# Kernel optimization log

Hardware: AMD Instinct MI355X
Metric: run time of the kernel (lower is better)

Reference implementation:

```python
import jax, jax.numpy as jnp
import numpy as np

CLASSES = (16, 16)
CH_IN = 128
CH_LAT = 128
B, H, W = 1, 192, 256


def setup_inputs() -> dict:
    key = jax.random.key(0)
    ks = jax.random.split(key, 20)

    def w(k, shape, fan_in):
        return (jax.random.normal(k, shape, jnp.float32) / np.float32(np.sqrt(fan_in)))

    c0, c1 = CLASSES
    inp = {
        "x_in": jax.random.normal(ks[0], (B, CH_IN, H, W), jnp.float32),
        # 1x1 convs: weight [out, in], bias [out]
        "w_c11": w(ks[1], (CH_LAT, CH_IN), CH_IN), "b_c11": 0.01 * jax.random.normal(ks[2], (CH_LAT,), jnp.float32),
        "w_c12": w(ks[3], (CH_LAT, CH_LAT), CH_LAT), "b_c12": 0.01 * jax.random.normal(ks[4], (CH_LAT,), jnp.float32),
        "w_c13": w(ks[5], (c0 + 1, CH_LAT), CH_LAT), "b_c13": 0.01 * jax.random.normal(ks[6], (c0 + 1,), jnp.float32),
        # CondMul: weight [n_classes, in, out], bias [n_classes, out]
        "w_c21": w(ks[7], (c0, CH_IN, 32), CH_IN), "b_c21": 0.01 * jax.random.normal(ks[8], (c0, 32), jnp.float32),
        "w_c22": w(ks[9], (c0, 32, 32), 32), "b_c22": 0.01 * jax.random.normal(ks[10], (c0, 32), jnp.float32),
        "w_c23": w(ks[11], (c0, 32, c1), 32), "b_c23": 0.01 * jax.random.normal(ks[12], (c0, c1), jnp.float32),
        "w_r11": w(ks[13], (c0 * c1, CH_IN, 32), CH_IN), "b_r11": 0.01 * jax.random.normal(ks[14], (c0 * c1, 32), jnp.float32),
        "w_r12": w(ks[15], (c0 * c1, 32, 16), 32), "b_r12": 0.01 * jax.random.normal(ks[16], (c0 * c1, 16), jnp.float32),
        "w_r13": w(ks[17], (c0 * c1, 16, 1), 16), "b_r13": 0.01 * jax.random.normal(ks[18], (c0 * c1, 1), jnp.float32),
    }
    return inp


def _conv1x1(x, w, b):
    # x: [B,C,H,W], w: [O,C] -> [B,O,H,W]
    return jnp.einsum('bchw,oc->bohw', x, w) + b[None, :, None, None]


def _cond_mul(x, inds, w, b):
    # x: [N,in], inds: [N] int32, w: [C,in,out], b: [C,out] -> [N,out]
    return jnp.einsum('ni,nio->no', x, w[inds]) + b[inds]


def reference(x_in, w_c11, b_c11, w_c12, b_c12, w_c13, b_c13,
              w_c21, b_c21, w_c22, b_c22, w_c23, b_c23,
              w_r11, b_r11, w_r12, b_r12, w_r13, b_r13):
    lrelu = jax.nn.leaky_relu  # negative_slope=0.01, matches F.leaky_relu default
    c0, c1 = CLASSES
    total = c0 * c1

    x1 = lrelu(_conv1x1(x_in, w_c11, b_c11))
    x1 = lrelu(_conv1x1(x1, w_c12, b_c12))
    x1 = _conv1x1(x1, w_c13, b_c13)  # [B, c0+1, H, W]
    mask = lrelu(x1[:, -1:, :, :])

    # coarse routing: argmax over class logits, flattened in (B,H,W) order as in torch
    inds1 = jnp.argmax(x1[:, :c0], axis=1).reshape(-1).astype(jnp.int32)

    # tokens flattened via transpose(1,3): (B,W,H) order, faithful to original
    tok = jnp.transpose(x_in, (0, 3, 2, 1)).reshape(-1, x_in.shape[1])  # [N, CH_IN]

    x2 = lrelu(_cond_mul(tok, inds1, w_c21, b_c21))
    x2 = lrelu(_cond_mul(x2, inds1, w_c22, b_c22))
    x2 = _cond_mul(x2, inds1, w_c23, b_c23)  # [N, c1]

    inds2 = jnp.argmax(x2, axis=1).astype(jnp.int32)
    inds12 = inds1 * c0 + inds2  # original multiplies by classes[0]

    x3 = lrelu(_cond_mul(tok, inds12, w_r11, b_r11))
    x3 = lrelu(_cond_mul(x3, inds12, w_r12, b_r12))
    r = _cond_mul(x3, inds12, w_r13, b_r13).reshape(-1)  # [N]

    x_real = (inds12.astype(jnp.float32) + r) * (1.0 / float(total))
    x_real = x_real.reshape(x_in.shape[0], 1, x_in.shape[2], x_in.shape[3])
    return x_real, mask
```

## Files before the change

### kernel.cpp

```cpp
#include <hip/hip_runtime.h>

#define NPIX 49152
#define H_ 192
#define W_ 256
#define TPB 64

__global__ __launch_bounds__(256) void wtrans2_k(const float* __restrict__ Wa,
    float* __restrict__ WTa, const float* __restrict__ Wb,
    float* __restrict__ WTb, int* __restrict__ S) {
  const int b = blockIdx.x;
  const float* __restrict__ W = (b < 16) ? Wa : Wb;
  float* __restrict__ WT = (b < 16) ? WTa : WTb;
  const int bb = b & 15;
  __shared__ float tile[32][33];
  const int bx = bb & 3, by = bb >> 2;
  const int c = threadIdx.x & 31, r0 = threadIdx.x >> 5;
#pragma unroll
  for (int j = 0; j < 4; ++j) {
    const int r = r0 + j * 8;
    tile[r][c] = W[(by * 32 + r) * 128 + bx * 32 + c];
  }
  __syncthreads();
#pragma unroll
  for (int j = 0; j < 4; ++j) {
    const int r = r0 + j * 8;
    WT[(bx * 32 + r) * 128 + by * 32 + c] = tile[c][r];
  }
  if (b == 0) {
    const int t = threadIdx.x;
    if (t < 32) S[t] = 0;
    S[1088 + t] = 0;
    S[1344 + t] = 0;
  }
}

__global__ __launch_bounds__(512) void convfused_k(const float* __restrict__ X,
    const float* __restrict__ WT1, const float* __restrict__ Bv1,
    const float* __restrict__ WT2, const float* __restrict__ Bv2,
    const float* __restrict__ W3, const float* __restrict__ Bv3,
    unsigned char* __restrict__ inds1, float* __restrict__ mask_out,
    int* __restrict__ cnt1, float* __restrict__ xt) {
  __shared__ float xs2[128][65];
  __shared__ float w3s[128 * 20];
  __shared__ int lh[16];
  const int t = threadIdx.x;
  const int px = t & 63;
  const int p0 = blockIdx.x * 64;
  int ob = (t >> 6) * 16;
  ob = __builtin_amdgcn_readfirstlane(ob);
  if (t < 16) lh[t] = 0;

  {
    float xr[16];
#pragma unroll
    for (int kk = 0; kk < 16; ++kk)
      xr[kk] = X[(ob + kk) * NPIX + p0 + px];
#pragma unroll
    for (int kk = 0; kk < 16; ++kk)
      xs2[ob + kk][px] = xr[kk];
  }
  __syncthreads();

  float acc[16];

  const float* __restrict__ W1u = WT1 + ob;
#pragma unroll
  for (int o = 0; o < 16; ++o) acc[o] = Bv1[ob + o];
#pragma unroll 8
  for (int k = 0; k < 128; ++k) {
    const float xv = xs2[k][px];
#pragma unroll
    for (int o = 0; o < 16; ++o)
      acc[o] = fmaf(xv, W1u[k * 128 + o], acc[o]);
  }

#pragma unroll
  for (int i = 0; i < 4; ++i) {
    const int idx = t * 4 + i;
    const int tok = idx >> 5, c4 = idx & 31;
    const int pg = p0 + tok;
    float4 v;
    v.x = xs2[c4 * 4 + 0][tok];
    v.y = xs2[c4 * 4 + 1][tok];
    v.z = xs2[c4 * 4 + 2][tok];
    v.w = xs2[c4 * 4 + 3][tok];
    *(float4*)(xt + ((pg & 255) * H_ + (pg >> 8)) * 128 + c4 * 4) = v;
  }
  __syncthreads();

#pragma unroll
  for (int o = 0; o < 16; ++o) {
    const float v = acc[o];
    xs2[ob + o][px] = v > 0.f ? v : 0.01f * v;
  }
  __syncthreads();

  const float* __restrict__ W2u = WT2 + ob;
#pragma unroll
  for (int o = 0; o < 16; ++o) acc[o] = Bv2[ob + o];
#pragma unroll 8
  for (int k = 0; k < 128; ++k) {
    const float xv = xs2[k][px];
#pragma unroll
    for (int o = 0; o < 16; ++o)
      acc[o] = fmaf(xv, W2u[k * 128 + o], acc[o]);
  }
  __syncthreads();

#pragma unroll
  for (int o = 0; o < 16; ++o) {
    const float v = acc[o];
    xs2[ob + o][px] = v > 0.f ? v : 0.01f * v;
  }
  for (int i = t; i < 17 * 128; i += 512)
    w3s[(i & 127) * 20 + (i >> 7)] = W3[i];
  __syncthreads();

  {
    const int p = t >> 3, s = t & 7;
    float s2[2];
    s2[0] = Bv3[2 * s];
    s2[1] = Bv3[2 * s + 1];
    float m = Bv3[16];
#pragma unroll 8
    for (int k = 0; k < 128; ++k) {
      const float xv = xs2[k][p];
      float2 w2 = *(const float2*)&w3s[k * 20 + 2 * s];
      s2[0] = fmaf(xv, w2.x, s2[0]);
      s2[1] = fmaf(xv, w2.y, s2[1]);
      m = fmaf(xv, w3s[k * 20 + 16], m);
    }
    float bv = s2[0];
    int bi = 2 * s;
    if (s2[1] > bv) { bv = s2[1]; bi = 2 * s + 1; }
#pragma unroll
    for (int d = 1; d < 8; d <<= 1) {
      const float ov = __shfl_xor(bv, d, 64);
      const int oi = __shfl_xor(bi, d, 64);
      if (ov > bv || (ov == bv && oi < bi)) { bv = ov; bi = oi; }
    }
    if (s == 0) {
      inds1[p0 + p] = (unsigned char)bi;
      mask_out[p0 + p] = m > 0.f ? m : 0.01f * m;
      atomicAdd(&lh[bi], 1);
    }
  }
  __syncthreads();
  if (t < 16 && lh[t] > 0) atomicAdd(&cnt1[t], lh[t]);
}

template<int NB>
__global__ __launch_bounds__(256) void scan_desc_k(const int* __restrict__ cnt,
    int* __restrict__ off, int* __restrict__ desc, int* __restrict__ ndesc) {
  const int t = threadIdx.x;
  const int lane = t & 63, wvi = t >> 6;
  __shared__ int wsumC[4], wsumD[4];
  const int c = (t < NB) ? cnt[t] : 0;
  const int nb = (c + TPB - 1) / TPB;
  int ic = c, id = nb;
  for (int d = 1; d < 64; d <<= 1) {
    const int uc = __shfl_up(ic, d, 64);
    const int ud = __shfl_up(id, d, 64);
    if (lane >= d) { ic += uc; id += ud; }
  }
  if (lane == 63) { wsumC[wvi] = ic; wsumD[wvi] = id; }
  __syncthreads();
  int bc = 0, bd = 0;
#pragma unroll
  for (int w2 = 0; w2 < 4; ++w2) {
    if (w2 < wvi) { bc += wsumC[w2]; bd += wsumD[w2]; }
  }
  ic += bc; id += bd;
  if (t < NB) {
    off[t] = ic - c;
    const int db = id - nb;
    for (int j = 0; j < nb; ++j) desc[db + j] = (t << 12) | j;
  }
  if (t == NB - 1) *ndesc = id;
}

template<typename T>
__global__ __launch_bounds__(256) void scatter_k(const T* __restrict__ bins,
    const int* __restrict__ off, int* __restrict__ cursor,
    int* __restrict__ ord, int nbins) {
  __shared__ int lhist[256], lbase[256], lcur[256];
  const int t = threadIdx.x;
  const int n = blockIdx.x * 256 + t;
  if (t < nbins) { lhist[t] = 0; lcur[t] = 0; }
  __syncthreads();
  const int b = (int)bins[n];
  atomicAdd(&lhist[b], 1);
  __syncthreads();
  if (t < nbins && lhist[t] > 0) lbase[t] = atomicAdd(&cursor[t], lhist[t]);
  __syncthreads();
  const int r = atomicAdd(&lcur[b], 1);
  ord[off[b] + lbase[b] + r] = n;
}

__global__ __launch_bounds__(256) void chain1_k(const float* __restrict__ xt,
    const int* __restrict__ ord1, const int* __restrict__ off1,
    const int* __restrict__ cnt1, const int* __restrict__ desc1,
    const int* __restrict__ nd1,
    const float* __restrict__ wc21, const float* __restrict__ bc21,
    const float* __restrict__ wc22, const float* __restrict__ bc22,
    const float* __restrict__ wc23, const float* __restrict__ bc23,
    int* __restrict__ e12a, int* __restrict__ cnt2) {
  if ((int)blockIdx.x >= *nd1) return;
  __shared__ float w1s[4096];
  __shared__ float w2s[1024];
  __shared__ float w3s[512];
  __shared__ float bs[80];
  __shared__ float xs_[64][132];
  __shared__ int lh[16];
  const int t = threadIdx.x;
  if (t < 16) lh[t] = 0;
  const int tg = t >> 2, sub = t & 3;
  const int l0 = (t & 63) & ~3;
  const int de = desc1[blockIdx.x];
  const int e = de >> 12, chunk = de & 0xFFF;
  const int cnt = cnt1[e];
  const int pos = chunk * TPB + tg;
  const bool valid = pos < cnt;
  const int n = valid ? ord1[off1[e] + pos] : 0;

  {
    const float4* __restrict__ Wg1 = (const float4*)(wc21 + e * 4096);
#pragma unroll
    for (int j = 0; j < 4; ++j)
      *(float4*)&w1s[t * 4 + j * 1024] = Wg1[t + j * 256];
    const float4* __restrict__ Wg2 = (const float4*)(wc22 + e * 1024);
    *(float4*)&w2s[t * 4] = Wg2[t];
    if (t < 128) {
      const float4* __restrict__ Wg3 = (const float4*)(wc23 + e * 512);
      *(float4*)&w3s[t * 4] = Wg3[t];
    }
    if (t < 32) bs[t] = bc21[e * 32 + t];
    else if (t < 64) bs[t] = bc22[e * 32 + (t - 32)];
    else if (t < 80) bs[t] = bc23[e * 16 + (t - 64)];
  }
  {
    const float4* __restrict__ src = (const float4*)(xt + n * 128 + sub * 32);
    float4 tmp[8];
#pragma unroll
    for (int j = 0; j < 8; ++j) tmp[j] = src[j];
#pragma unroll
    for (int j = 0; j < 8; ++j)
      *(float4*)(&xs_[tg][sub * 32 + 4 * j]) = tmp[j];
  }
  __syncthreads();

  const int wb1 = sub * 8;
  float a[8];
#pragma unroll
  for (int o = 0; o < 8; ++o) a[o] = bs[wb1 + o];
#pragma unroll
  for (int k = 0; k < 128; k += 4) {
    float x4[4];
    *(float4*)x4 = *(const float4*)(&xs_[tg][k]);
#pragma unroll
    for (int kk = 0; kk < 4; ++kk) {
      float w8[8];
      *(float4*)&w8[0] = *(const float4*)&w1s[(k + kk) * 32 + wb1];
      *(float4*)&w8[4] = *(const float4*)&w1s[(k + kk) * 32 + wb1 + 4];
#pragma unroll
      for (int o = 0; o < 8; ++o) a[o] = fmaf(x4[kk], w8[o], a[o]);
    }
  }
#pragma unroll
  for (int o = 0; o < 8; ++o) a[o] = a[o] > 0.f ? a[o] : 0.01f * a[o];

  float b[8];
#pragma unroll
  for (int o = 0; o < 8; ++o) b[o] = bs[32 + wb1 + o];
#pragma unroll
  for (int i = 0; i < 32; ++i) {
    const float hv = __shfl(a[i & 7], l0 + (i >> 3), 64);
    float w8[8];
    *(float4*)&w8[0] = *(const float4*)&w2s[i * 32 + wb1];
    *(float4*)&w8[4] = *(const float4*)&w2s[i * 32 + wb1 + 4];
#pragma unroll
    for (int o = 0; o < 8; ++o) b[o] = fmaf(hv, w8[o], b[o]);
  }
#pragma unroll
  for (int o = 0; o < 8; ++o) b[o] = b[o] > 0.f ? b[o] : 0.01f * b[o];

  float s[4];
#pragma unroll
  for (int j = 0; j < 4; ++j) s[j] = bs[64 + sub * 4 + j];
#pragma unroll
  for (int i = 0; i < 32; ++i) {
    const float hv = __shfl(b[i & 7], l0 + (i >> 3), 64);
    float w4[4];
    *(float4*)w4 = *(const float4*)&w3s[i * 16 + sub * 4];
#pragma unroll
    for (int j = 0; j < 4; ++j) s[j] = fmaf(hv, w4[j], s[j]);
  }

  float bv = s[0];
  int bi = sub * 4;
#pragma unroll
  for (int j = 1; j < 4; ++j) {
    if (s[j] > bv) { bv = s[j]; bi = sub * 4 + j; }
  }
#pragma unroll
  for (int d = 1; d < 4; d <<= 1) {
    const float ov = __shfl_xor(bv, d, 64);
    const int oi = __shfl_xor(bi, d, 64);
    if (ov > bv || (ov == bv && oi < bi)) { bv = ov; bi = oi; }
  }
  const int e12 = e * 16 + bi;
  if (valid && sub == 0) {
    e12a[n] = e12;
    atomicAdd(&lh[bi], 1);
  }
  __syncthreads();
  if (t < 16 && lh[t] > 0)
    atomicAdd(&cnt2[e * 16 + t], lh[t]);
}

__global__ __launch_bounds__(256) void chain2_k(const float* __restrict__ xt,
    const int* __restrict__ ord2, const int* __restrict__ off2,
    const int* __restrict__ cnt2, const int* __restrict__ desc2,
    const int* __restrict__ nd2,
    const float* __restrict__ wr11, const float* __restrict__ br11,
    const float* __restrict__ wr12, const float* __restrict__ br12,
    const float* __restrict__ wr13, const float* __restrict__ br13,
    float* __restrict__ out) {
  if ((int)blockIdx.x >= *nd2) return;
  __shared__ float w1s[4096];
  __shared__ float w2s[512];
  __shared__ float w3s[16];
  __shared__ float bs[49];
  __shared__ float xs_[64][132];
  const int t = threadIdx.x;
  const int tg = t >> 2, sub = t & 3;
  const int l0 = (t & 63) & ~3;
  const int de = desc2[blockIdx.x];
  const int e12 = de >> 12, chunk = de & 0xFFF;
  const int cnt = cnt2[e12];
  const int pos = chunk * TPB + tg;
  const bool valid = pos < cnt;
  const int n = valid ? ord2[off2[e12] + pos] : 0;

  {
    const float4* __restrict__ Wg1 = (const float4*)(wr11 + e12 * 4096);
#pragma unroll
    for (int j = 0; j < 4; ++j)
      *(float4*)&w1s[t * 4 + j * 1024] = Wg1[t + j * 256];
    if (t < 128) {
      const float4* __restrict__ Wg2 = (const float4*)(wr12 + e12 * 512);
      *(float4*)&w2s[t * 4] = Wg2[t];
    }
    if (t < 16) w3s[t] = wr13[e12 * 16 + t];
    if (t < 32) bs[t] = br11[e12 * 32 + t];
    else if (t < 48) bs[t] = br12[e12 * 16 + (t - 32)];
    else if (t == 48) bs[48] = br13[e12];
  }
  {
    const float4* __restrict__ src = (const float4*)(xt + n * 128 + sub * 32);
    float4 tmp[8];
#pragma unroll
    for (int j = 0; j < 8; ++j) tmp[j] = src[j];
#pragma unroll
    for (int j = 0; j < 8; ++j)
      *(float4*)(&xs_[tg][sub * 32 + 4 * j]) = tmp[j];
  }
  __syncthreads();

  const int wb1 = sub * 8;
  float a[8];
#pragma unroll
  for (int o = 0; o < 8; ++o) a[o] = bs[wb1 + o];
#pragma unroll
  for (int k = 0; k < 128; k += 4) {
    float x4[4];
    *(float4*)x4 = *(const float4*)(&xs_[tg][k]);
#pragma unroll
    for (int kk = 0; kk < 4; ++kk) {
      float w8[8];
      *(float4*)&w8[0] = *(const float4*)&w1s[(k + kk) * 32 + wb1];
      *(float4*)&w8[4] = *(const float4*)&w1s[(k + kk) * 32 + wb1 + 4];
#pragma unroll
      for (int o = 0; o < 8; ++o) a[o] = fmaf(x4[kk], w8[o], a[o]);
    }
  }
#pragma unroll
  for (int o = 0; o < 8; ++o) a[o] = a[o] > 0.f ? a[o] : 0.01f * a[o];

  float s[4];
#pragma unroll
  for (int j = 0; j < 4; ++j) s[j] = bs[32 + sub * 4 + j];
#pragma unroll
  for (int i = 0; i < 32; ++i) {
    const float hv = __shfl(a[i & 7], l0 + (i >> 3), 64);
    float w4[4];
    *(float4*)w4 = *(const float4*)&w2s[i * 16 + sub * 4];
#pragma unroll
    for (int j = 0; j < 4; ++j) s[j] = fmaf(hv, w4[j], s[j]);
  }
#pragma unroll
  for (int j = 0; j < 4; ++j) s[j] = s[j] > 0.f ? s[j] : 0.01f * s[j];

  float r = bs[48];
#pragma unroll
  for (int i = 0; i < 16; ++i) {
    const float hv = __shfl(s[i & 3], l0 + (i >> 2), 64);
    r = fmaf(hv, w3s[i], r);
  }

  if (valid && sub == 0) out[n] = ((float)e12 + r) * (1.0f / 256.0f);
}

extern "C" void kernel_launch(void* const* d_in, const int* in_sizes, int n_in,
                              void* d_out, int out_size, void* d_ws,
                              size_t ws_size, hipStream_t stream) {
  const float* x_in  = (const float*)d_in[0];
  const float* w_c11 = (const float*)d_in[1];
  const float* b_c11 = (const float*)d_in[2];
  const float* w_c12 = (const float*)d_in[3];
  const float* b_c12 = (const float*)d_in[4];
  const float* w_c13 = (const float*)d_in[5];
  const float* b_c13 = (const float*)d_in[6];
  const float* w_c21 = (const float*)d_in[7];
  const float* b_c21 = (const float*)d_in[8];
  const float* w_c22 = (const float*)d_in[9];
  const float* b_c22 = (const float*)d_in[10];
  const float* w_c23 = (const float*)d_in[11];
  const float* b_c23 = (const float*)d_in[12];
  const float* w_r11 = (const float*)d_in[13];
  const float* b_r11 = (const float*)d_in[14];
  const float* w_r12 = (const float*)d_in[15];
  const float* b_r12 = (const float*)d_in[16];
  const float* w_r13 = (const float*)d_in[17];
  const float* b_r13 = (const float*)d_in[18];

  float* out = (float*)d_out;

  float* R0 = (float*)d_ws;
  float* R1 = R0 + 128 * NPIX;
  float* R2 = R1 + 128 * NPIX;

  float* xt = R0;
  unsigned char* inds1 = (unsigned char*)R2;
  float* wT1 = R2 + 12288;
  float* wT2 = wT1 + 16384;
  int* S = (int*)R2 + 45056;

  int* cnt1  = S;
  int* cur1  = S + 16;
  int* off1  = S + 32;
  int* nd1   = S + 48;
  int* desc1 = S + 64;
  int* cnt2  = S + 1088;
  int* cur2  = S + 1344;
  int* off2  = S + 1600;
  int* nd2   = S + 1856;
  int* desc2 = S + 1872;

  int* ib   = (int*)R1;
  int* ord1 = ib;
  int* ord2 = ib + NPIX;
  int* e12a = ib + 2 * NPIX;

  wtrans2_k<<<32, 256, 0, stream>>>(w_c11, wT1, w_c12, wT2, S);
  convfused_k<<<NPIX / 64, 512, 0, stream>>>(x_in, wT1, b_c11, wT2, b_c12,
      w_c13, b_c13, inds1, out + NPIX, cnt1, xt);
  scan_desc_k<16><<<1, 256, 0, stream>>>(cnt1, off1, desc1, nd1);
  scatter_k<unsigned char><<<NPIX / 256, 256, 0, stream>>>(inds1, off1, cur1,
                                                           ord1, 16);
  chain1_k<<<NPIX / TPB + 16, 256, 0, stream>>>(xt, ord1, off1, cnt1, desc1,
      nd1, w_c21, b_c21, w_c22, b_c22, w_c23, b_c23, e12a, cnt2);
  scan_desc_k<256><<<1, 256, 0, stream>>>(cnt2, off2, desc2, nd2);
  scatter_k<int><<<NPIX / 256, 256, 0, stream>>>(e12a, off2, cur2, ord2, 256);
  chain2_k<<<NPIX / TPB + 256, 256, 0, stream>>>(xt, ord2, off2, cnt2, desc2,
      nd2, w_r11, b_r11, w_r12, b_r12, w_r13, b_r13, out);
}
```

Measured before the change: 123.0 us.

## Restructure cond-MLP kernels to wave-uniform weight loads with transposed token tiles

Both routed MLP kernels now map one token per lane and one output slice per wavefront. Because the wave index is made uniform with readfirstlane, weights can be read straight from global memory as scalar loads instead of being staged into LDS. Activations move between layers through padded transposed LDS tiles, which replaces the cross-lane shuffles. This cuts the LDS footprint and the per-block weight staging, at the cost of more barriers and a serial 16-way argmax done by a single wave.

```diff
diff --git a/kernel.cpp b/kernel.cpp
--- a/kernel.cpp
+++ b/kernel.cpp
@@ -206,112 +206,103 @@
     const float* __restrict__ wc23, const float* __restrict__ bc23,
     int* __restrict__ e12a, int* __restrict__ cnt2) {
   if ((int)blockIdx.x >= *nd1) return;
-  __shared__ float w1s[4096];
-  __shared__ float w2s[1024];
-  __shared__ float w3s[512];
-  __shared__ float bs[80];
-  __shared__ float xs_[64][132];
+  __shared__ float xs_t[128][65];
+  __shared__ float actA[32][65];
+  __shared__ float actB[32][65];
   __shared__ int lh[16];
   const int t = threadIdx.x;
   if (t < 16) lh[t] = 0;
-  const int tg = t >> 2, sub = t & 3;
-  const int l0 = (t & 63) & ~3;
+  const int tok = t & 63;
+  int w = t >> 6;
+  w = __builtin_amdgcn_readfirstlane(w);
   const int de = desc1[blockIdx.x];
   const int e = de >> 12, chunk = de & 0xFFF;
   const int cnt = cnt1[e];
-  const int pos = chunk * TPB + tg;
+  const int pos = chunk * TPB + tok;
   const bool valid = pos < cnt;
   const int n = valid ? ord1[off1[e] + pos] : 0;
 
   {
-    const float4* __restrict__ Wg1 = (const float4*)(wc21 + e * 4096);
+    const float4* __restrict__ src = (const float4*)(xt + n * 128 + w * 32);
+    float4 tmp[8];
+#pragma unroll
+    for (int j = 0; j < 8; ++j) tmp[j] = src[j];
+#pragma unroll
+    for (int j = 0; j < 8; ++j) {
+      const float* v = (const float*)&tmp[j];
+#pragma unroll
+      for (int c = 0; c < 4; ++c)
+        xs_t[w * 32 + j * 4 + c][tok] = v[c];
+    }
+  }
+  __syncthreads();
+
+  const float* __restrict__ W1u = wc21 + e * 4096 + w * 8;
+  const float* __restrict__ B1u = bc21 + e * 32 + w * 8;
+  float a[8];
+#pragma unroll
+  for (int o = 0; o < 8; ++o) a[o] = B1u[o];
+#pragma unroll 8
+  for (int k = 0; k < 128; ++k) {
+    const float xv = xs_t[k][tok];
+#pragma unroll
+    for (int o = 0; o < 8; ++o)
+      a[o] = fmaf(xv, W1u[k * 32 + o], a[o]);
+  }
+#pragma unroll
+  for (int o = 0; o < 8; ++o) {
+    const float v = a[o] > 0.f ? a[o] : 0.01f * a[o];
+    actA[w * 8 + o][tok] = v;
+  }
+  __syncthreads();
+
+  const float* __restrict__ W2u = wc22 + e * 1024 + w * 8;
+  const float* __restrict__ B2u = bc22 + e * 32 + w * 8;
+  float b[8];
+#pragma unroll
+  for (int o = 0; o < 8; ++o) b[o] = B2u[o];
+#pragma unroll 8
+  for (int i = 0; i < 32; ++i) {
+    const float hv = actA[i][tok];
+#pragma unroll
+    for (int o = 0; o < 8; ++o)
+      b[o] = fmaf(hv, W2u[i * 32 + o], b[o]);
+  }
+#pragma unroll
+  for (int o = 0; o < 8; ++o) {
+    const float v = b[o] > 0.f ? b[o] : 0.01f * b[o];
+    actB[w * 8 + o][tok] = v;
+  }
+  __syncthreads();
+
+  const float* __restrict__ W3u = wc23 + e * 512 + w * 4;
+  const float* __restrict__ B3u = bc23 + e * 16 + w * 4;
+  float s[4];
+#pragma unroll
+  for (int j = 0; j < 4; ++j) s[j] = B3u[j];
+#pragma unroll 8
+  for (int i = 0; i < 32; ++i) {
+    const float hv = actB[i][tok];
 #pragma unroll
     for (int j = 0; j < 4; ++j)
-      *(float4*)&w1s[t * 4 + j * 1024] = Wg1[t + j * 256];
-    const float4* __restrict__ Wg2 = (const float4*)(wc22 + e * 1024);
-    *(float4*)&w2s[t * 4] = Wg2[t];
-    if (t < 128) {
-      const float4* __restrict__ Wg3 = (const float4*)(wc23 + e * 512);
-      *(float4*)&w3s[t * 4] = Wg3[t];
-    }
-    if (t < 32) bs[t] = bc21[e * 32 + t];
-    else if (t < 64) bs[t] = bc22[e * 32 + (t - 32)];
-    else if (t < 80) bs[t] = bc23[e * 16 + (t - 64)];
-  }
-  {
-    const float4* __restrict__ src = (const float4*)(xt + n * 128 + sub * 32);
-    float4 tmp[8];
-#pragma unroll
-    for (int j = 0; j < 8; ++j) tmp[j] = src[j];
-#pragma unroll
-    for (int j = 0; j < 8; ++j)
-      *(float4*)(&xs_[tg][sub * 32 + 4 * j]) = tmp[j];
-  }
-  __syncthreads();
-
-  const int wb1 = sub * 8;
-  float a[8];
-#pragma unroll
-  for (int o = 0; o < 8; ++o) a[o] = bs[wb1 + o];
-#pragma unroll
-  for (int k = 0; k < 128; k += 4) {
-    float x4[4];
-    *(float4*)x4 = *(const float4*)(&xs_[tg][k]);
-#pragma unroll
-    for (int kk = 0; kk < 4; ++kk) {
-      float w8[8];
-      *(float4*)&w8[0] = *(const float4*)&w1s[(k + kk) * 32 + wb1];
-      *(float4*)&w8[4] = *(const float4*)&w1s[(k + kk) * 32 + wb1 + 4];
-#pragma unroll
-      for (int o = 0; o < 8; ++o) a[o] = fmaf(x4[kk], w8[o], a[o]);
-    }
-  }
-#pragma unroll
-  for (int o = 0; o < 8; ++o) a[o] = a[o] > 0.f ? a[o] : 0.01f * a[o];
-
-  float b[8];
-#pragma unroll
-  for (int o = 0; o < 8; ++o) b[o] = bs[32 + wb1 + o];
-#pragma unroll
-  for (int i = 0; i < 32; ++i) {
-    const float hv = __shfl(a[i & 7], l0 + (i >> 3), 64);
-    float w8[8];
-    *(float4*)&w8[0] = *(const float4*)&w2s[i * 32 + wb1];
-    *(float4*)&w8[4] = *(const float4*)&w2s[i * 32 + wb1 + 4];
-#pragma unroll
-    for (int o = 0; o < 8; ++o) b[o] = fmaf(hv, w8[o], b[o]);
-  }
-#pragma unroll
-  for (int o = 0; o < 8; ++o) b[o] = b[o] > 0.f ? b[o] : 0.01f * b[o];
-
-  float s[4];
-#pragma unroll
-  for (int j = 0; j < 4; ++j) s[j] = bs[64 + sub * 4 + j];
-#pragma unroll
-  for (int i = 0; i < 32; ++i) {
-    const float hv = __shfl(b[i & 7], l0 + (i >> 3), 64);
-    float w4[4];
-    *(float4*)w4 = *(const float4*)&w3s[i * 16 + sub * 4];
-#pragma unroll
-    for (int j = 0; j < 4; ++j) s[j] = fmaf(hv, w4[j], s[j]);
-  }
-
-  float bv = s[0];
-  int bi = sub * 4;
-#pragma unroll
-  for (int j = 1; j < 4; ++j) {
-    if (s[j] > bv) { bv = s[j]; bi = sub * 4 + j; }
-  }
-#pragma unroll
-  for (int d = 1; d < 4; d <<= 1) {
-    const float ov = __shfl_xor(bv, d, 64);
-    const int oi = __shfl_xor(bi, d, 64);
-    if (ov > bv || (ov == bv && oi < bi)) { bv = ov; bi = oi; }
-  }
-  const int e12 = e * 16 + bi;
-  if (valid && sub == 0) {
-    e12a[n] = e12;
-    atomicAdd(&lh[bi], 1);
+      s[j] = fmaf(hv, W3u[i * 16 + j], s[j]);
+  }
+#pragma unroll
+  for (int j = 0; j < 4; ++j) actA[w * 4 + j][tok] = s[j];
+  __syncthreads();
+
+  if (t < 64) {
+    float bv = actA[0][tok];
+    int am = 0;
+#pragma unroll
+    for (int o = 1; o < 16; ++o) {
+      const float v = actA[o][tok];
+      if (v > bv) { bv = v; am = o; }
+    }
+    if (valid) {
+      e12a[n] = e * 16 + am;
+      atomicAdd(&lh[am], 1);
+    }
   }
   __syncthreads();
   if (t < 16 && lh[t] > 0)
@@ -327,88 +318,81 @@
     const float* __restrict__ wr13, const float* __restrict__ br13,
     float* __restrict__ out) {
   if ((int)blockIdx.x >= *nd2) return;
-  __shared__ float w1s[4096];
-  __shared__ float w2s[512];
-  __shared__ float w3s[16];
-  __shared__ float bs[49];
-  __shared__ float xs_[64][132];
+  __shared__ float xs_t[128][65];
+  __shared__ float actA[32][65];
+  __shared__ float actB[16][65];
   const int t = threadIdx.x;
-  const int tg = t >> 2, sub = t & 3;
-  const int l0 = (t & 63) & ~3;
+  const int tok = t & 63;
+  int w = t >> 6;
+  w = __builtin_amdgcn_readfirstlane(w);
   const int de = desc2[blockIdx.x];
   const int e12 = de >> 12, chunk = de & 0xFFF;
   const int cnt = cnt2[e12];
-  const int pos = chunk * TPB + tg;
+  const int pos = chunk * TPB + tok;
   const bool valid = pos < cnt;
   const int n = valid ? ord2[off2[e12] + pos] : 0;
 
   {
-    const float4* __restrict__ Wg1 = (const float4*)(wr11 + e12 * 4096);
+    const float4* __restrict__ src = (const float4*)(xt + n * 128 + w * 32);
+    float4 tmp[8];
+#pragma unroll
+    for (int j = 0; j < 8; ++j) tmp[j] = src[j];
+#pragma unroll
+    for (int j = 0; j < 8; ++j) {
+      const float* v = (const float*)&tmp[j];
+#pragma unroll
+      for (int c = 0; c < 4; ++c)
+        xs_t[w * 32 + j * 4 + c][tok] = v[c];
+    }
+  }
+  __syncthreads();
+
+  const float* __restrict__ W1u = wr11 + e12 * 4096 + w * 8;
+  const float* __restrict__ B1u = br11 + e12 * 32 + w * 8;
+  float a[8];
+#pragma unroll
+  for (int o = 0; o < 8; ++o) a[o] = B1u[o];
+#pragma unroll 8
+  for (int k = 0; k < 128; ++k) {
+    const float xv = xs_t[k][tok];
+#pragma unroll
+    for (int o = 0; o < 8; ++o)
+      a[o] = fmaf(xv, W1u[k * 32 + o], a[o]);
+  }
+#pragma unroll
+  for (int o = 0; o < 8; ++o) {
+    const float v = a[o] > 0.f ? a[o] : 0.01f * a[o];
+    actA[w * 8 + o][tok] = v;
+  }
+  __syncthreads();
+
+  const float* __restrict__ W2u = wr12 + e12 * 512 + w * 4;
+  const float* __restrict__ B2u = br12 + e12 * 16 + w * 4;
+  float s[4];
+#pragma unroll
+  for (int j = 0; j < 4; ++j) s[j] = B2u[j];
+#pragma unroll 8
+  for (int i = 0; i < 32; ++i) {
+    const float hv = actA[i][tok];
 #pragma unroll
     for (int j = 0; j < 4; ++j)
-      *(float4*)&w1s[t * 4 + j * 1024] = Wg1[t + j * 256];
-    if (t < 128) {
-      const float4* __restrict__ Wg2 = (const float4*)(wr12 + e12 * 512);
-      *(float4*)&w2s[t * 4] = Wg2[t];
-    }
-    if (t < 16) w3s[t] = wr13[e12 * 16 + t];
-    if (t < 32) bs[t] = br11[e12 * 32 + t];
-    else if (t < 48) bs[t] = br12[e12 * 16 + (t - 32)];
-    else if (t == 48) bs[48] = br13[e12];
-  }
-  {
-    const float4* __restrict__ src = (const float4*)(xt + n * 128 + sub * 32);
-    float4 tmp[8];
-#pragma unroll
-    for (int j = 0; j < 8; ++j) tmp[j] = src[j];
-#pragma unroll
-    for (int j = 0; j < 8; ++j)
-      *(float4*)(&xs_[tg][sub * 32 + 4 * j]) = tmp[j];
-  }
-  __syncthreads();
-
-  const int wb1 = sub * 8;
-  float a[8];
-#pragma unroll
-  for (int o = 0; o < 8; ++o) a[o] = bs[wb1 + o];
-#pragma unroll
-  for (int k = 0; k < 128; k += 4) {
-    float x4[4];
-    *(float4*)x4 = *(const float4*)(&xs_[tg][k]);
-#pragma unroll
-    for (int kk = 0; kk < 4; ++kk) {
-      float w8[8];
-      *(float4*)&w8[0] = *(const float4*)&w1s[(k + kk) * 32 + wb1];
-      *(float4*)&w8[4] = *(const float4*)&w1s[(k + kk) * 32 + wb1 + 4];
-#pragma unroll
-      for (int o = 0; o < 8; ++o) a[o] = fmaf(x4[kk], w8[o], a[o]);
-    }
-  }
-#pragma unroll
-  for (int o = 0; o < 8; ++o) a[o] = a[o] > 0.f ? a[o] : 0.01f * a[o];
-
-  float s[4];
-#pragma unroll
-  for (int j = 0; j < 4; ++j) s[j] = bs[32 + sub * 4 + j];
-#pragma unroll
-  for (int i = 0; i < 32; ++i) {
-    const float hv = __shfl(a[i & 7], l0 + (i >> 3), 64);
-    float w4[4];
-    *(float4*)w4 = *(const float4*)&w2s[i * 16 + sub * 4];
-#pragma unroll
-    for (int j = 0; j < 4; ++j) s[j] = fmaf(hv, w4[j], s[j]);
-  }
-#pragma unroll
-  for (int j = 0; j < 4; ++j) s[j] = s[j] > 0.f ? s[j] : 0.01f * s[j];
-
-  float r = bs[48];
-#pragma unroll
-  for (int i = 0; i < 16; ++i) {
-    const float hv = __shfl(s[i & 3], l0 + (i >> 2), 64);
-    r = fmaf(hv, w3s[i], r);
-  }
-
-  if (valid && sub == 0) out[n] = ((float)e12 + r) * (1.0f / 256.0f);
+      s[j] = fmaf(hv, W2u[i * 16 + j], s[j]);
+  }
+#pragma unroll
+  for (int j = 0; j < 4; ++j) {
+    const float v = s[j] > 0.f ? s[j] : 0.01f * s[j];
+    actB[w * 4 + j][tok] = v;
+  }
+  __syncthreads();
+
+  if (t < 64) {
+    float r = br13[e12];
+    const float* __restrict__ W3u = wr13 + e12 * 16;
+#pragma unroll
+    for (int i = 0; i < 16; ++i)
+      r = fmaf(actB[i][tok], W3u[i], r);
+    if (valid) out[n] = ((float)e12 + r) * (1.0f / 256.0f);
+  }
 }
 
 extern "C" void kernel_launch(void* const* d_in, const int* in_sizes, int n_in,
```

Measured after the change: 144.4 us. 1.17x slower.

## Fold per-expert prefix scans into scatter and chain kernels, drop scan launches

Applied to the files above, without the earlier changes.

Removes the two single-block scan_desc kernels. Each scatter block and each chain block now recomputes the exclusive prefix sum of the expert counts itself, and chain blocks find their expert and chunk by comparing blockIdx against the scanned block counts. This cuts two serial launches and their descriptor and offset global traffic from the dependency chain. In exchange every block repeats a small 256-wide scan, which adds an extra __syncthreads and the cnt loads.

```diff
diff --git a/kernel.cpp b/kernel.cpp
--- a/kernel.cpp
+++ b/kernel.cpp
@@ -149,79 +149,91 @@
   if (t < 16 && lh[t] > 0) atomicAdd(&cnt1[t], lh[t]);
 }
 
-template<int NB>
-__global__ __launch_bounds__(256) void scan_desc_k(const int* __restrict__ cnt,
-    int* __restrict__ off, int* __restrict__ desc, int* __restrict__ ndesc) {
+template<typename T>
+__global__ __launch_bounds__(256) void scatter_k(const T* __restrict__ bins,
+    const int* __restrict__ cnt, int* __restrict__ cursor,
+    int* __restrict__ ord, int nbins) {
+  __shared__ int loff[256], lhist[256], lbase[256], lcur[256];
+  __shared__ int wsC[4];
   const int t = threadIdx.x;
   const int lane = t & 63, wvi = t >> 6;
-  __shared__ int wsumC[4], wsumD[4];
-  const int c = (t < NB) ? cnt[t] : 0;
-  const int nb = (c + TPB - 1) / TPB;
-  int ic = c, id = nb;
+  const int c = (t < nbins) ? cnt[t] : 0;
+  int ic = c;
   for (int d = 1; d < 64; d <<= 1) {
-    const int uc = __shfl_up(ic, d, 64);
-    const int ud = __shfl_up(id, d, 64);
-    if (lane >= d) { ic += uc; id += ud; }
-  }
-  if (lane == 63) { wsumC[wvi] = ic; wsumD[wvi] = id; }
-  __syncthreads();
-  int bc = 0, bd = 0;
-#pragma unroll
-  for (int w2 = 0; w2 < 4; ++w2) {
-    if (w2 < wvi) { bc += wsumC[w2]; bd += wsumD[w2]; }
-  }
-  ic += bc; id += bd;
-  if (t < NB) {
-    off[t] = ic - c;
-    const int db = id - nb;
-    for (int j = 0; j < nb; ++j) desc[db + j] = (t << 12) | j;
-  }
-  if (t == NB - 1) *ndesc = id;
-}
-
-template<typename T>
-__global__ __launch_bounds__(256) void scatter_k(const T* __restrict__ bins,
-    const int* __restrict__ off, int* __restrict__ cursor,
-    int* __restrict__ ord, int nbins) {
-  __shared__ int lhist[256], lbase[256], lcur[256];
-  const int t = threadIdx.x;
+    const int u = __shfl_up(ic, d, 64);
+    if (lane >= d) ic += u;
+  }
+  if (lane == 63) wsC[wvi] = ic;
+  if (t < nbins) { lhist[t] = 0; lcur[t] = 0; }
+  __syncthreads();
+  int bc = 0;
+#pragma unroll
+  for (int w2 = 0; w2 < 4; ++w2) if (w2 < wvi) bc += wsC[w2];
+  ic += bc;
+  if (t < nbins) loff[t] = ic - c;
+  __syncthreads();
   const int n = blockIdx.x * 256 + t;
-  if (t < nbins) { lhist[t] = 0; lcur[t] = 0; }
-  __syncthreads();
   const int b = (int)bins[n];
   atomicAdd(&lhist[b], 1);
   __syncthreads();
   if (t < nbins && lhist[t] > 0) lbase[t] = atomicAdd(&cursor[t], lhist[t]);
   __syncthreads();
   const int r = atomicAdd(&lcur[b], 1);
-  ord[off[b] + lbase[b] + r] = n;
+  ord[loff[b] + lbase[b] + r] = n;
 }
 
 __global__ __launch_bounds__(256) void chain1_k(const float* __restrict__ xt,
-    const int* __restrict__ ord1, const int* __restrict__ off1,
-    const int* __restrict__ cnt1, const int* __restrict__ desc1,
-    const int* __restrict__ nd1,
+    const int* __restrict__ ord1, const int* __restrict__ cnt1,
     const float* __restrict__ wc21, const float* __restrict__ bc21,
     const float* __restrict__ wc22, const float* __restrict__ bc22,
     const float* __restrict__ wc23, const float* __restrict__ bc23,
     int* __restrict__ e12a, int* __restrict__ cnt2) {
-  if ((int)blockIdx.x >= *nd1) return;
   __shared__ float w1s[4096];
   __shared__ float w2s[1024];
   __shared__ float w3s[512];
   __shared__ float bs[80];
   __shared__ float xs_[64][132];
   __shared__ int lh[16];
+  __shared__ int sel[4];
+  __shared__ int wsC[4], wsD[4];
   const int t = threadIdx.x;
+  const int lane = t & 63, wvi = t >> 6;
+  if (t == 0) sel[0] = -1;
   if (t < 16) lh[t] = 0;
+  {
+    const int cb = (t < 16) ? cnt1[t] : 0;
+    const int nb = (cb + TPB - 1) / TPB;
+    int ic = cb, id = nb;
+    for (int d = 1; d < 64; d <<= 1) {
+      const int uc = __shfl_up(ic, d, 64);
+      const int ud = __shfl_up(id, d, 64);
+      if (lane >= d) { ic += uc; id += ud; }
+    }
+    if (lane == 63) { wsC[wvi] = ic; wsD[wvi] = id; }
+    __syncthreads();
+    int bc = 0, bd = 0;
+#pragma unroll
+    for (int w2 = 0; w2 < 4; ++w2) {
+      if (w2 < wvi) { bc += wsC[w2]; bd += wsD[w2]; }
+    }
+    ic += bc; id += bd;
+    const int accB = id - nb, accO = ic - cb;
+    if (t < 16 && (int)blockIdx.x >= accB && (int)blockIdx.x < accB + nb) {
+      sel[0] = t; sel[1] = blockIdx.x - accB; sel[2] = accO; sel[3] = cb;
+    }
+  }
+  __syncthreads();
+  if (sel[0] < 0) return;
+  const int e     = __builtin_amdgcn_readfirstlane(sel[0]);
+  const int chunk = __builtin_amdgcn_readfirstlane(sel[1]);
+  const int offe  = __builtin_amdgcn_readfirstlane(sel[2]);
+  const int cnt   = __builtin_amdgcn_readfirstlane(sel[3]);
+
   const int tg = t >> 2, sub = t & 3;
   const int l0 = (t & 63) & ~3;
-  const int de = desc1[blockIdx.x];
-  const int e = de >> 12, chunk = de & 0xFFF;
-  const int cnt = cnt1[e];
   const int pos = chunk * TPB + tg;
   const bool valid = pos < cnt;
-  const int n = valid ? ord1[off1[e] + pos] : 0;
+  const int n = valid ? ord1[offe + pos] : 0;
 
   {
     const float4* __restrict__ Wg1 = (const float4*)(wc21 + e * 4096);
@@ -319,28 +331,55 @@
 }
 
 __global__ __launch_bounds__(256) void chain2_k(const float* __restrict__ xt,
-    const int* __restrict__ ord2, const int* __restrict__ off2,
-    const int* __restrict__ cnt2, const int* __restrict__ desc2,
-    const int* __restrict__ nd2,
+    const int* __restrict__ ord2, const int* __restrict__ cnt2,
     const float* __restrict__ wr11, const float* __restrict__ br11,
     const float* __restrict__ wr12, const float* __restrict__ br12,
     const float* __restrict__ wr13, const float* __restrict__ br13,
     float* __restrict__ out) {
-  if ((int)blockIdx.x >= *nd2) return;
   __shared__ float w1s[4096];
   __shared__ float w2s[512];
   __shared__ float w3s[16];
   __shared__ float bs[49];
   __shared__ float xs_[64][132];
+  __shared__ int sel[4];
+  __shared__ int wsC[4], wsD[4];
   const int t = threadIdx.x;
+  const int lane = t & 63, wvi = t >> 6;
+  if (t == 0) sel[0] = -1;
+  {
+    const int cb = cnt2[t];
+    const int nb = (cb + TPB - 1) / TPB;
+    int ic = cb, id = nb;
+    for (int d = 1; d < 64; d <<= 1) {
+      const int uc = __shfl_up(ic, d, 64);
+      const int ud = __shfl_up(id, d, 64);
+      if (lane >= d) { ic += uc; id += ud; }
+    }
+    if (lane == 63) { wsC[wvi] = ic; wsD[wvi] = id; }
+    __syncthreads();
+    int bc = 0, bd = 0;
+#pragma unroll
+    for (int w2 = 0; w2 < 4; ++w2) {
+      if (w2 < wvi) { bc += wsC[w2]; bd += wsD[w2]; }
+    }
+    ic += bc; id += bd;
+    const int accB = id - nb, accO = ic - cb;
+    if ((int)blockIdx.x >= accB && (int)blockIdx.x < accB + nb) {
+      sel[0] = t; sel[1] = blockIdx.x - accB; sel[2] = accO; sel[3] = cb;
+    }
+  }
+  __syncthreads();
+  if (sel[0] < 0) return;
+  const int e12   = __builtin_amdgcn_readfirstlane(sel[0]);
+  const int chunk = __builtin_amdgcn_readfirstlane(sel[1]);
+  const int offe  = __builtin_amdgcn_readfirstlane(sel[2]);
+  const int cnt   = __builtin_amdgcn_readfirstlane(sel[3]);
+
   const int tg = t >> 2, sub = t & 3;
   const int l0 = (t & 63) & ~3;
-  const int de = desc2[blockIdx.x];
-  const int e12 = de >> 12, chunk = de & 0xFFF;
-  const int cnt = cnt2[e12];
   const int pos = chunk * TPB + tg;
   const bool valid = pos < cnt;
-  const int n = valid ? ord2[off2[e12] + pos] : 0;
+  const int n = valid ? ord2[offe + pos] : 0;
 
   {
     const float4* __restrict__ Wg1 = (const float4*)(wr11 + e12 * 4096);
@@ -446,16 +485,10 @@
   float* wT2 = wT1 + 16384;
   int* S = (int*)R2 + 45056;
 
-  int* cnt1  = S;
-  int* cur1  = S + 16;
-  int* off1  = S + 32;
-  int* nd1   = S + 48;
-  int* desc1 = S + 64;
-  int* cnt2  = S + 1088;
-  int* cur2  = S + 1344;
-  int* off2  = S + 1600;
-  int* nd2   = S + 1856;
-  int* desc2 = S + 1872;
+  int* cnt1 = S;
+  int* cur1 = S + 16;
+  int* cnt2 = S + 1088;
+  int* cur2 = S + 1344;
 
   int* ib   = (int*)R1;
   int* ord1 = ib;
@@ -465,13 +498,11 @@
   wtrans2_k<<<32, 256, 0, stream>>>(w_c11, wT1, w_c12, wT2, S);
   convfused_k<<<NPIX / 64, 512, 0, stream>>>(x_in, wT1, b_c11, wT2, b_c12,
       w_c13, b_c13, inds1, out + NPIX, cnt1, xt);
-  scan_desc_k<16><<<1, 256, 0, stream>>>(cnt1, off1, desc1, nd1);
-  scatter_k<unsigned char><<<NPIX / 256, 256, 0, stream>>>(inds1, off1, cur1,
+  scatter_k<unsigned char><<<NPIX / 256, 256, 0, stream>>>(inds1, cnt1, cur1,
                                                            ord1, 16);
-  chain1_k<<<NPIX / TPB + 16, 256, 0, stream>>>(xt, ord1, off1, cnt1, desc1,
-      nd1, w_c21, b_c21, w_c22, b_c22, w_c23, b_c23, e12a, cnt2);
-  scan_desc_k<256><<<1, 256, 0, stream>>>(cnt2, off2, desc2, nd2);
-  scatter_k<int><<<NPIX / 256, 256, 0, stream>>>(e12a, off2, cur2, ord2, 256);
-  chain2_k<<<NPIX / TPB + 256, 256, 0, stream>>>(xt, ord2, off2, cnt2, desc2,
-      nd2, w_r11, b_r11, w_r12, b_r12, w_r13, b_r13, out);
+  chain1_k<<<NPIX / TPB + 16, 256, 0, stream>>>(xt, ord1, cnt1,
+      w_c21, b_c21, w_c22, b_c22, w_c23, b_c23, e12a, cnt2);
+  scatter_k<int><<<NPIX / 256, 256, 0, stream>>>(e12a, cnt2, cur2, ord2, 256);
+  chain2_k<<<NPIX / TPB + 256, 256, 0, stream>>>(xt, ord2, cnt2,
+      w_r11, b_r11, w_r12, b_r12, w_r13, b_r13, out);
 }
```

Result: faster. 115.3 us, median of 3 (-6.2%).
